# Kernel optimization log

Hardware: AMD Instinct MI355X
Metric: run time of the kernel (lower is better)

Reference implementation:

```python
import jax, jax.numpy as jnp
import numpy as np

LN_EPS = 1e-5
BN_EPS = 1e-5
ALPHA = 0.1

def _layer_norm(x):
    # F.layer_norm over last dim, no affine
    mu = jnp.mean(x, axis=-1, keepdims=True)
    var = jnp.var(x, axis=-1, keepdims=True)
    return (x - mu) * jax.lax.rsqrt(var + LN_EPS)

def setup_inputs() -> dict:
    key = jax.random.key(0)
    ks = jax.random.split(key, 12)
    N, Nh, D, Dq = 8192, 8192, 64, 64
    s = 1.0 / np.sqrt(D)
    inp = {
        "X": jax.random.normal(ks[0], (N, D), jnp.float32),
        "H": jax.random.normal(ks[1], (Nh, D), jnp.float32),
        "M": jax.random.uniform(ks[2], (N, Nh), jnp.float32),
        # Linear params (torch nn.Linear: y = x @ W.T + b), uniform init scale
        "Qw": jax.random.uniform(ks[3], (Dq, D), jnp.float32, -s, s),
        "Qb": jax.random.uniform(ks[4], (Dq,), jnp.float32, -s, s),
        "Kw": jax.random.uniform(ks[5], (Dq, D), jnp.float32, -s, s),
        "Kb": jax.random.uniform(ks[6], (Dq,), jnp.float32, -s, s),
        "Vw": jax.random.uniform(ks[7], (64, D), jnp.float32, -s, s),
        "Vb": jax.random.uniform(ks[8], (64,), jnp.float32, -s, s),
        # BatchNorm1d(64) eval-mode params
        "bn_gamma": jnp.ones((64,), jnp.float32),
        "bn_beta": jnp.zeros((64,), jnp.float32),
        "bn_mean": 0.1 * jax.random.normal(ks[9], (64,), jnp.float32),
        "bn_var": jax.random.uniform(ks[10], (64,), jnp.float32, 0.5, 1.5),
    }
    return inp

def reference(X, H, M, Qw, Qb, Kw, Kb, Vw, Vb, bn_gamma, bn_beta, bn_mean, bn_var):
    # K/Q branches: Linear + LayerNorm
    K = _layer_norm(H @ Kw.T + Kb)            # [Nh, Dq]
    Q = _layer_norm(X @ Qw.T + Qb)            # [N, Dq]
    # V branch: Linear + BatchNorm1d (eval mode; dropout is identity in eval)
    V = (H @ Vw.T + Vb - bn_mean) * jax.lax.rsqrt(bn_var + BN_EPS) * bn_gamma + bn_beta  # [Nh, 64]
    # Masked attention, softmax over dim=0 (columns)
    A = (Q @ K.T) * 0.125                     # [N, Nh]
    A = jax.nn.softmax(M * A, axis=0)
    # globel=True branch
    return ALPHA * (A @ V) + M @ H            # [N, 64]
```

## Files before the change

### kernel.cpp

```cpp
#include <hip/hip_runtime.h>
#include <hip/hip_bf16.h>
#include <math.h>

#define NN 8192
#define QSCALE (0.125f * 1.44269504088896f)
#define OSZ (8192*64)

typedef __attribute__((ext_vector_type(8))) short short8;
typedef __attribute__((ext_vector_type(16))) float f32x16;
typedef __attribute__((ext_vector_type(4))) unsigned uint4e;

union W4 { uint4e u4; unsigned u[4]; short8 v; };

__device__ inline unsigned short f2bf(float x) {
  union { float f; unsigned u; } t; t.f = x;
  unsigned r = t.u + 0x7fffu + ((t.u >> 16) & 1u);
  return (unsigned short)(r >> 16);
}
__device__ inline unsigned cvtpk(float lo, float hi) {
  unsigned r;
  asm("v_cvt_pk_bf16_f32 %0, %1, %2" : "=v"(r) : "v"(lo), "v"(hi));
  return r;
}

__global__ __launch_bounds__(256) void qkv_kernel(
    const float* __restrict__ X, const float* __restrict__ H,
    const float* __restrict__ Qw, const float* __restrict__ Qb,
    const float* __restrict__ Kw, const float* __restrict__ Kb,
    const float* __restrict__ Vw, const float* __restrict__ Vb,
    const float* __restrict__ bng, const float* __restrict__ bnb,
    const float* __restrict__ bnm, const float* __restrict__ bnv,
    unsigned short* __restrict__ QP, unsigned short* __restrict__ KP,
    unsigned short* __restrict__ VP, unsigned short* __restrict__ HP)
{
  int wid = (blockIdx.x * blockDim.x + threadIdx.x) >> 6;
  int d = threadIdx.x & 63;
  float4 w[16];

  for (int fq = 0; fq < 16; fq++) w[fq] = *(const float4*)(Qw + d*64 + fq*4);
  for (int rr = 0; rr < 4; rr++) {
    int r = wid*4 + rr;
    float a = Qb[d];
    for (int fq = 0; fq < 16; fq++) {
      float4 xv = *(const float4*)(X + r*64 + fq*4);
      a += w[fq].x*xv.x + w[fq].y*xv.y + w[fq].z*xv.z + w[fq].w*xv.w;
    }
    float s = a;
    for (int off = 32; off; off >>= 1) s += __shfl_xor(s, off);
    float mean = s * (1.f/64.f);
    float c = a - mean;
    float s2 = c*c;
    for (int off = 32; off; off >>= 1) s2 += __shfl_xor(s2, off);
    float q = c * rsqrtf(s2*(1.f/64.f) + 1e-5f);
    QP[(d>>3)*65536 + r*8 + (d&7)] = f2bf(q * QSCALE);
  }
  for (int fq = 0; fq < 16; fq++) w[fq] = *(const float4*)(Kw + d*64 + fq*4);
  for (int rr = 0; rr < 4; rr++) {
    int r = wid*4 + rr;
    float a = Kb[d];
    for (int fq = 0; fq < 16; fq++) {
      float4 hv = *(const float4*)(H + r*64 + fq*4);
      a += w[fq].x*hv.x + w[fq].y*hv.y + w[fq].z*hv.z + w[fq].w*hv.w;
    }
    float s = a;
    for (int off = 32; off; off >>= 1) s += __shfl_xor(s, off);
    float mean = s * (1.f/64.f);
    float c = a - mean;
    float s2 = c*c;
    for (int off = 32; off; off >>= 1) s2 += __shfl_xor(s2, off);
    float k = c * rsqrtf(s2*(1.f/64.f) + 1e-5f);
    KP[(d>>3)*65536 + r*8 + (d&7)] = f2bf(k);
  }
  for (int fq = 0; fq < 16; fq++) w[fq] = *(const float4*)(Vw + d*64 + fq*4);
  float bscale = rsqrtf(bnv[d] + 1e-5f) * bng[d];
  for (int rr = 0; rr < 4; rr++) {
    int r = wid*4 + rr;
    float a = Vb[d];
    for (int fq = 0; fq < 16; fq++) {
      float4 hv = *(const float4*)(H + r*64 + fq*4);
      a += w[fq].x*hv.x + w[fq].y*hv.y + w[fq].z*hv.z + w[fq].w*hv.w;
    }
    float v = (a - bnm[d]) * bscale + bnb[d];
    VP[(r>>3)*512 + d*8 + (r&7)] = f2bf(v);
    HP[(r>>3)*512 + d*8 + (r&7)] = f2bf(H[r*64 + d]);
  }
}

__global__ __launch_bounds__(256) void pass1_kernel(
    const float* __restrict__ M, const unsigned short* __restrict__ QP,
    const unsigned short* __restrict__ KP, unsigned* __restrict__ MT4,
    float* __restrict__ pd)
{
  __shared__ __align__(16) float ld[4][32*34];
  int tid = threadIdx.x;
  int wj = (blockIdx.x * blockDim.x + tid) >> 6;
  int lane = tid & 63;
  int wv = tid >> 6;
  int l31 = lane & 31, h = lane >> 5;
  int jb = wj & 255, slice = wj >> 8;
  int j = jb*32 + l31;
  float* lds = ld[wv];

  short8 kb[4];
  for (int m = 0; m < 4; m++)
    kb[m] = *(const short8*)(KP + (2*m + h)*65536 + j*8);

  float Mv[16];
  {
    int i0 = slice*8*32;
#pragma unroll
    for (int r = 0; r < 16; r++) {
      int ir = (r&3) + 8*(r>>2) + 4*h;
      Mv[r] = __builtin_nontemporal_load(M + (size_t)(i0 + ir)*NN + j);
    }
  }

  float d0 = 0.f, d1 = 0.f, d2 = 0.f, d3 = 0.f;
  for (int t = 0; t < 8; t++) {
    int i0 = (slice*8 + t) * 32;
    float Mn[16];
    if (t < 7) {
      int i1 = i0 + 32;
#pragma unroll
      for (int r = 0; r < 16; r++) {
        int ir = (r&3) + 8*(r>>2) + 4*h;
        Mn[r] = __builtin_nontemporal_load(M + (size_t)(i1 + ir)*NN + j);
      }
    }

    f32x16 acc;
    for (int r = 0; r < 16; r++) acc[r] = 0.f;
    for (int m = 0; m < 4; m++) {
      short8 qa = *(const short8*)(QP + (2*m + h)*65536 + (size_t)(i0 + l31)*8);
      acc = __builtin_amdgcn_mfma_f32_32x32x16_bf16(qa, kb[m], acc, 0, 0, 0);
    }

#pragma unroll
    for (int r = 0; r < 16; r++) {
      int ir = (r&3) + 8*(r>>2) + 4*h;
      lds[ir*34 + l31] = Mv[r];
    }
    d0 += exp2f(acc[0]*Mv[0]) + exp2f(acc[4]*Mv[4]) + exp2f(acc[8]*Mv[8])   + exp2f(acc[12]*Mv[12]);
    d1 += exp2f(acc[1]*Mv[1]) + exp2f(acc[5]*Mv[5]) + exp2f(acc[9]*Mv[9])   + exp2f(acc[13]*Mv[13]);
    d2 += exp2f(acc[2]*Mv[2]) + exp2f(acc[6]*Mv[6]) + exp2f(acc[10]*Mv[10]) + exp2f(acc[14]*Mv[14]);
    d3 += exp2f(acc[3]*Mv[3]) + exp2f(acc[7]*Mv[7]) + exp2f(acc[11]*Mv[11]) + exp2f(acc[15]*Mv[15]);

    asm volatile("s_waitcnt lgkmcnt(0)" ::: "memory");
    int ii = l31;
    int i_g = i0 + ii;
#pragma unroll
    for (int qq = 0; qq < 2; qq++) {
      int q = 2*h + qq;
      unsigned w0, w1, w2, w3;
      {
        float2 a2 = *(const float2*)(&lds[ii*34 + 8*q + 0]);
        float2 b2 = *(const float2*)(&lds[ii*34 + 8*q + 2]);
        float2 c2 = *(const float2*)(&lds[ii*34 + 8*q + 4]);
        float2 e2 = *(const float2*)(&lds[ii*34 + 8*q + 6]);
        w0 = cvtpk(a2.x, a2.y); w1 = cvtpk(b2.x, b2.y);
        w2 = cvtpk(c2.x, c2.y); w3 = cvtpk(e2.x, e2.y);
      }
      uint4e ww = {w0, w1, w2, w3};
      *(uint4e*)(MT4 + (size_t)(jb*4 + q)*32768 + (size_t)i_g*4) = ww;
    }
    if (t < 7) {
#pragma unroll
      for (int r = 0; r < 16; r++) Mv[r] = Mn[r];
    }
  }
  float drun = (d0 + d1) + (d2 + d3);
  drun += __shfl_xor(drun, 32);
  if (lane < 32) pd[(size_t)slice*NN + j] = drun;
}

__global__ __launch_bounds__(256) void combine_kernel(
    const float* __restrict__ pd, float* __restrict__ colcc)
{
  int j = blockIdx.x * blockDim.x + threadIdx.x;
  float Dv = 0.f;
  for (int s = 0; s < 32; s++) Dv += pd[(size_t)s*NN + j];
  colcc[j] = log2f(Dv * 10.f);
}

__global__ __launch_bounds__(256) void pass2_kernel(
    const unsigned* __restrict__ MT4, const unsigned short* __restrict__ QP,
    const unsigned short* __restrict__ KP, const unsigned short* __restrict__ VP,
    const unsigned short* __restrict__ HP, const float* __restrict__ colcc,
    float* __restrict__ opart)
{
  __shared__ __align__(16) float cls[512];

  int iblk = blockIdx.x >> 4, slice = blockIdx.x & 15;
  int i0 = iblk * 64;
  int tid = threadIdx.x;
  int lane = tid & 63, wid = tid >> 6;
  int l31 = lane & 31, h = lane >> 5;
  int iq = wid & 1, dh = wid >> 1;
  int row = iq*32 + l31;
  int i_g = i0 + row;

  short8 qb[4];
  for (int m = 0; m < 4; m++)
    qb[m] = *(const short8*)(QP + (2*m + h)*65536 + (size_t)i_g*8);

  cls[tid]       = colcc[slice*512 + tid];
  cls[tid + 256] = colcc[slice*512 + 256 + tid];
  __syncthreads();

  f32x16 oacc;
  for (int r = 0; r < 16; r++) oacc[r] = 0.f;

  const unsigned* mbase = MT4 + (size_t)i_g*4;

  W4 A0c, A1c; short8 kac[4];
  {
    int jt = slice*512, jtb = jt >> 3;
    A0c.u4 = *(const uint4e*)(mbase + (size_t)(jtb + h)*32768);
    A1c.u4 = *(const uint4e*)(mbase + (size_t)(jtb + 2 + h)*32768);
    for (int m = 0; m < 4; m++)
      kac[m] = *(const short8*)(KP + (2*m + h)*65536 + (size_t)(jt + l31)*8);
  }

  for (int t = 0; t < 16; t++) {
    int jt = slice*512 + t*32;

    W4 A0n, A1n; short8 kan[4];
    if (t < 15) {
      int jn = jt + 32, jnb = jn >> 3;
      A0n.u4 = *(const uint4e*)(mbase + (size_t)(jnb + h)*32768);
      A1n.u4 = *(const uint4e*)(mbase + (size_t)(jnb + 2 + h)*32768);
      for (int m = 0; m < 4; m++)
        kan[m] = *(const short8*)(KP + (2*m + h)*65536 + (size_t)(jn + l31)*8);
    }

    int j8 = jt >> 3;
    const unsigned short* vbase = VP + (size_t)j8*512 + (dh*32 + l31)*8;
    const unsigned short* hbase = HP + (size_t)j8*512 + (dh*32 + l31)*8;
    short8 vb1 = *(const short8*)(vbase + h*512);
    short8 vb2 = *(const short8*)(vbase + (2 + h)*512);
    short8 hb1 = *(const short8*)(hbase + h*512);
    short8 hb2 = *(const short8*)(hbase + (2 + h)*512);

    f32x16 sacc;
    for (int r = 0; r < 16; r++) sacc[r] = 0.f;
    for (int m = 0; m < 4; m++)
      sacc = __builtin_amdgcn_mfma_f32_32x32x16_bf16(kac[m], qb[m], sacc, 0, 0, 0);

    unsigned mw0 = A0c.u[0], mw2 = A0c.u[2];
    unsigned mw1 = A0c.u[1], mw3 = A0c.u[3];
    unsigned mw4 = A1c.u[0], mw6 = A1c.u[2];
    unsigned mw5 = A1c.u[1], mw7 = A1c.u[3];
    asm volatile("v_permlane32_swap_b32 %0, %1" : "+v"(mw0), "+v"(mw2));
    asm volatile("v_permlane32_swap_b32 %0, %1" : "+v"(mw1), "+v"(mw3));
    asm volatile("v_permlane32_swap_b32 %0, %1" : "+v"(mw4), "+v"(mw6));
    asm volatile("v_permlane32_swap_b32 %0, %1" : "+v"(mw5), "+v"(mw7));
    unsigned mw[8] = {mw0, mw1, mw2, mw3, mw4, mw5, mw6, mw7};

    float p[16];
#pragma unroll
    for (int q = 0; q < 4; q++) {
      float4 cc = *(const float4*)(&cls[t*32 + 8*q + 4*h]);
      unsigned wa = mw[2*q], wb = mw[2*q + 1];
      float m0 = __uint_as_float(wa << 16);
      float m1 = __uint_as_float(wa & 0xffff0000u);
      float m2 = __uint_as_float(wb << 16);
      float m3 = __uint_as_float(wb & 0xffff0000u);
      p[4*q+0] = exp2f(fmaf(sacc[4*q+0], m0, -cc.x));
      p[4*q+1] = exp2f(fmaf(sacc[4*q+1], m1, -cc.y));
      p[4*q+2] = exp2f(fmaf(sacc[4*q+2], m2, -cc.z));
      p[4*q+3] = exp2f(fmaf(sacc[4*q+3], m3, -cc.w));
    }
    unsigned pu[8];
#pragma unroll
    for (int k = 0; k < 8; k++) pu[k] = cvtpk(p[2*k], p[2*k+1]);

    asm volatile("v_permlane32_swap_b32 %0, %1" : "+v"(pu[0]), "+v"(pu[2]));
    asm volatile("v_permlane32_swap_b32 %0, %1" : "+v"(pu[1]), "+v"(pu[3]));
    asm volatile("v_permlane32_swap_b32 %0, %1" : "+v"(pu[4]), "+v"(pu[6]));
    asm volatile("v_permlane32_swap_b32 %0, %1" : "+v"(pu[5]), "+v"(pu[7]));

    W4 PA0, PA1;
    PA0.u[0] = pu[0]; PA0.u[1] = pu[1]; PA0.u[2] = pu[2]; PA0.u[3] = pu[3];
    PA1.u[0] = pu[4]; PA1.u[1] = pu[5]; PA1.u[2] = pu[6]; PA1.u[3] = pu[7];

    oacc = __builtin_amdgcn_mfma_f32_32x32x16_bf16(PA0.v, vb1, oacc, 0, 0, 0);
    oacc = __builtin_amdgcn_mfma_f32_32x32x16_bf16(PA1.v, vb2, oacc, 0, 0, 0);
    oacc = __builtin_amdgcn_mfma_f32_32x32x16_bf16(A0c.v, hb1, oacc, 0, 0, 0);
    oacc = __builtin_amdgcn_mfma_f32_32x32x16_bf16(A1c.v, hb2, oacc, 0, 0, 0);

    if (t < 15) {
      A0c = A1n;
    }
    if (t < 15) {
      A0c = A0n; A1c = A1n;
      for (int m = 0; m < 4; m++) kac[m] = kan[m];
    }
  }

  float* obase = opart + (size_t)slice*OSZ;
#pragma unroll
  for (int r = 0; r < 16; r++) {
    int orow = i0 + iq*32 + (r&3) + 8*(r>>2) + 4*h;
    int ocol = dh*32 + l31;
    obase[(size_t)orow*64 + ocol] = oacc[r];
  }
}

__global__ __launch_bounds__(256) void reduce_kernel(
    const float* __restrict__ opart, float* __restrict__ out)
{
  int e4 = blockIdx.x * blockDim.x + threadIdx.x;
  const float4* p = (const float4*)opart;
  float4 a = p[e4];
#pragma unroll
  for (int s = 1; s < 16; s++) {
    float4 b = p[(size_t)s*(OSZ/4) + e4];
    a.x += b.x; a.y += b.y; a.z += b.z; a.w += b.w;
  }
  ((float4*)out)[e4] = a;
}

extern "C" void kernel_launch(void* const* d_in, const int* in_sizes, int n_in,
                              void* d_out, int out_size, void* d_ws, size_t ws_size,
                              hipStream_t stream) {
  const float* X   = (const float*)d_in[0];
  const float* H   = (const float*)d_in[1];
  const float* M   = (const float*)d_in[2];
  const float* Qw  = (const float*)d_in[3];
  const float* Qb  = (const float*)d_in[4];
  const float* Kw  = (const float*)d_in[5];
  const float* Kb  = (const float*)d_in[6];
  const float* Vw  = (const float*)d_in[7];
  const float* Vb  = (const float*)d_in[8];
  const float* bng = (const float*)d_in[9];
  const float* bnb = (const float*)d_in[10];
  const float* bnm = (const float*)d_in[11];
  const float* bnv = (const float*)d_in[12];
  float* out = (float*)d_out;

  char* ws = (char*)d_ws;
  const size_t MB = 1024*1024;
  unsigned* MT4       = (unsigned*)(ws);
  unsigned short* QP  = (unsigned short*)(ws + 128*MB);
  unsigned short* KP  = (unsigned short*)(ws + 129*MB);
  unsigned short* VP  = (unsigned short*)(ws + 130*MB);
  unsigned short* HP  = (unsigned short*)(ws + 131*MB);
  float* pd           = (float*)(ws + 132*MB);
  float* colcc        = (float*)(ws + 133*MB);
  float* opart        = (float*)(ws + 134*MB);

  qkv_kernel<<<512, 256, 0, stream>>>(X, H, Qw, Qb, Kw, Kb, Vw, Vb,
                                      bng, bnb, bnm, bnv, QP, KP, VP, HP);
  pass1_kernel<<<2048, 256, 0, stream>>>(M, QP, KP, MT4, pd);
  combine_kernel<<<32, 256, 0, stream>>>(pd, colcc);
  pass2_kernel<<<2048, 256, 0, stream>>>(MT4, QP, KP, VP, HP, colcc, opart);
  reduce_kernel<<<512, 256, 0, stream>>>(opart, out);
}
```

Before: 200.8 us.

## Stage M tiles cooperatively in shared LDS with double buffering; use raw v_exp_f32

```diff
diff --git a/kernel.cpp b/kernel.cpp
--- a/kernel.cpp
+++ b/kernel.cpp
@@ -20,6 +20,11 @@
 __device__ inline unsigned cvtpk(float lo, float hi) {
   unsigned r;
   asm("v_cvt_pk_bf16_f32 %0, %1, %2" : "=v"(r) : "v"(lo), "v"(hi));
+  return r;
+}
+__device__ inline float fexp2(float x) {
+  float r;
+  asm("v_exp_f32 %0, %1" : "=v"(r) : "v"(x));
   return r;
 }
 
@@ -86,47 +91,55 @@
   }
 }
 
+#define MSTRIDE 132
+
 __global__ __launch_bounds__(256) void pass1_kernel(
     const float* __restrict__ M, const unsigned short* __restrict__ QP,
     const unsigned short* __restrict__ KP, unsigned* __restrict__ MT4,
     float* __restrict__ pd)
 {
-  __shared__ __align__(16) float ld[4][32*34];
+  __shared__ __align__(16) float mstage[2][32*MSTRIDE];
   int tid = threadIdx.x;
-  int wj = (blockIdx.x * blockDim.x + tid) >> 6;
   int lane = tid & 63;
   int wv = tid >> 6;
   int l31 = lane & 31, h = lane >> 5;
-  int jb = wj & 255, slice = wj >> 8;
+  int jb0 = (blockIdx.x*4) & 255;
+  int slice = blockIdx.x >> 6;
+  int jb = jb0 + wv;
   int j = jb*32 + l31;
-  float* lds = ld[wv];
 
   short8 kb[4];
   for (int m = 0; m < 4; m++)
     kb[m] = *(const short8*)(KP + (2*m + h)*65536 + j*8);
 
-  float Mv[16];
-  {
-    int i0 = slice*8*32;
-#pragma unroll
-    for (int r = 0; r < 16; r++) {
-      int ir = (r&3) + 8*(r>>2) + 4*h;
-      Mv[r] = __builtin_nontemporal_load(M + (size_t)(i0 + ir)*NN + j);
-    }
-  }
+  const float* msrc = M + (size_t)(slice*256)*NN + jb0*32;
+  int srow[4], scol[4];
+#pragma unroll
+  for (int rr = 0; rr < 4; rr++) {
+    int n = rr*256 + tid;
+    srow[rr] = n >> 5; scol[rr] = (n & 31) * 4;
+  }
+
+#pragma unroll
+  for (int rr = 0; rr < 4; rr++) {
+    float4 v = *(const float4*)(msrc + (size_t)srow[rr]*NN + scol[rr]);
+    *(float4*)(&mstage[0][srow[rr]*MSTRIDE + scol[rr]]) = v;
+  }
+  __syncthreads();
 
   float d0 = 0.f, d1 = 0.f, d2 = 0.f, d3 = 0.f;
   for (int t = 0; t < 8; t++) {
     int i0 = (slice*8 + t) * 32;
-    float Mn[16];
     if (t < 7) {
-      int i1 = i0 + 32;
-#pragma unroll
-      for (int r = 0; r < 16; r++) {
-        int ir = (r&3) + 8*(r>>2) + 4*h;
-        Mn[r] = __builtin_nontemporal_load(M + (size_t)(i1 + ir)*NN + j);
+      const float* src = msrc + (size_t)(t+1)*32*NN;
+      float* dst = mstage[(t+1) & 1];
+#pragma unroll
+      for (int rr = 0; rr < 4; rr++) {
+        float4 v = *(const float4*)(src + (size_t)srow[rr]*NN + scol[rr]);
+        *(float4*)(&dst[srow[rr]*MSTRIDE + scol[rr]]) = v;
       }
     }
+    const float* mb = mstage[t & 1];
 
     f32x16 acc;
     for (int r = 0; r < 16; r++) acc[r] = 0.f;
@@ -135,38 +148,32 @@
       acc = __builtin_amdgcn_mfma_f32_32x32x16_bf16(qa, kb[m], acc, 0, 0, 0);
     }
 
+    float Mv[16];
 #pragma unroll
     for (int r = 0; r < 16; r++) {
       int ir = (r&3) + 8*(r>>2) + 4*h;
-      lds[ir*34 + l31] = Mv[r];
-    }
-    d0 += exp2f(acc[0]*Mv[0]) + exp2f(acc[4]*Mv[4]) + exp2f(acc[8]*Mv[8])   + exp2f(acc[12]*Mv[12]);
-    d1 += exp2f(acc[1]*Mv[1]) + exp2f(acc[5]*Mv[5]) + exp2f(acc[9]*Mv[9])   + exp2f(acc[13]*Mv[13]);
-    d2 += exp2f(acc[2]*Mv[2]) + exp2f(acc[6]*Mv[6]) + exp2f(acc[10]*Mv[10]) + exp2f(acc[14]*Mv[14]);
-    d3 += exp2f(acc[3]*Mv[3]) + exp2f(acc[7]*Mv[7]) + exp2f(acc[11]*Mv[11]) + exp2f(acc[15]*Mv[15]);
-
-    asm volatile("s_waitcnt lgkmcnt(0)" ::: "memory");
+      Mv[r] = mb[ir*MSTRIDE + wv*32 + l31];
+    }
+    d0 += fexp2(acc[0]*Mv[0]) + fexp2(acc[4]*Mv[4]) + fexp2(acc[8]*Mv[8])   + fexp2(acc[12]*Mv[12]);
+    d1 += fexp2(acc[1]*Mv[1]) + fexp2(acc[5]*Mv[5]) + fexp2(acc[9]*Mv[9])   + fexp2(acc[13]*Mv[13]);
+    d2 += fexp2(acc[2]*Mv[2]) + fexp2(acc[6]*Mv[6]) + fexp2(acc[10]*Mv[10]) + fexp2(acc[14]*Mv[14]);
+    d3 += fexp2(acc[3]*Mv[3]) + fexp2(acc[7]*Mv[7]) + fexp2(acc[11]*Mv[11]) + fexp2(acc[15]*Mv[15]);
+
     int ii = l31;
     int i_g = i0 + ii;
 #pragma unroll
     for (int qq = 0; qq < 2; qq++) {
       int q = 2*h + qq;
-      unsigned w0, w1, w2, w3;
-      {
-        float2 a2 = *(const float2*)(&lds[ii*34 + 8*q + 0]);
-        float2 b2 = *(const float2*)(&lds[ii*34 + 8*q + 2]);
-        float2 c2 = *(const float2*)(&lds[ii*34 + 8*q + 4]);
-        float2 e2 = *(const float2*)(&lds[ii*34 + 8*q + 6]);
-        w0 = cvtpk(a2.x, a2.y); w1 = cvtpk(b2.x, b2.y);
-        w2 = cvtpk(c2.x, c2.y); w3 = cvtpk(e2.x, e2.y);
-      }
-      uint4e ww = {w0, w1, w2, w3};
+      const float* rbase = &mb[ii*MSTRIDE + wv*32 + 8*q];
+      float2 a2 = *(const float2*)(rbase + 0);
+      float2 b2 = *(const float2*)(rbase + 2);
+      float2 c2 = *(const float2*)(rbase + 4);
+      float2 e2 = *(const float2*)(rbase + 6);
+      uint4e ww = {cvtpk(a2.x, a2.y), cvtpk(b2.x, b2.y),
+                   cvtpk(c2.x, c2.y), cvtpk(e2.x, e2.y)};
       *(uint4e*)(MT4 + (size_t)(jb*4 + q)*32768 + (size_t)i_g*4) = ww;
     }
-    if (t < 7) {
-#pragma unroll
-      for (int r = 0; r < 16; r++) Mv[r] = Mn[r];
-    }
+    __syncthreads();
   }
   float drun = (d0 + d1) + (d2 + d3);
   drun += __shfl_xor(drun, 32);
@@ -265,10 +272,10 @@
       float m1 = __uint_as_float(wa & 0xffff0000u);
       float m2 = __uint_as_float(wb << 16);
       float m3 = __uint_as_float(wb & 0xffff0000u);
-      p[4*q+0] = exp2f(fmaf(sacc[4*q+0], m0, -cc.x));
-      p[4*q+1] = exp2f(fmaf(sacc[4*q+1], m1, -cc.y));
-      p[4*q+2] = exp2f(fmaf(sacc[4*q+2], m2, -cc.z));
-      p[4*q+3] = exp2f(fmaf(sacc[4*q+3], m3, -cc.w));
+      p[4*q+0] = fexp2(fmaf(sacc[4*q+0], m0, -cc.x));
+      p[4*q+1] = fexp2(fmaf(sacc[4*q+1], m1, -cc.y));
+      p[4*q+2] = fexp2(fmaf(sacc[4*q+2], m2, -cc.z));
+      p[4*q+3] = fexp2(fmaf(sacc[4*q+3], m3, -cc.w));
     }
     unsigned pu[8];
 #pragma unroll
@@ -288,9 +295,6 @@
     oacc = __builtin_amdgcn_mfma_f32_32x32x16_bf16(A0c.v, hb1, oacc, 0, 0, 0);
     oacc = __builtin_amdgcn_mfma_f32_32x32x16_bf16(A1c.v, hb2, oacc, 0, 0, 0);
 
-    if (t < 15) {
-      A0c = A1n;
-    }
     if (t < 15) {
       A0c = A0n; A1c = A1n;
       for (int m = 0; m < 4; m++) kac[m] = kan[m];
```

Measured after the change: 195.4 us. -2.7%, faster.
